# Kernel optimization log

Measured on AMD Instinct MI355X. Metric: run time of the kernel, lower is better.

## Reference

```python
import jax, jax.numpy as jnp
import numpy as np

EPS = 1e-6
LOG_2PI = float(np.log(2.0 * np.pi))


def setup_inputs() -> dict:
    key = jax.random.key(0)
    k1, k2 = jax.random.split(key)
    z = jax.random.normal(k1, (8, 32, 256, 256), dtype=jnp.float32)
    g = jax.random.uniform(k2, (8, 5, 256, 256), dtype=jnp.float32)
    return {"z": z, "g": g}


def _gmm_energy(z, g):
    b, c, h, w = z.shape
    k = g.shape[1]
    hw = h * w
    zf = z.reshape(b, c, hw)
    gf = g.reshape(b, k, hw)

    # phi: mean responsibility per component, [b, k]
    phi = jnp.sum(gf, axis=2) / hw

    # mu: weighted mean, then l2-normalized over channels, [b, k, c]
    gz = jnp.einsum('bkn,bcn->bkc', gf, zf)
    mu = gz / (jnp.sum(gf, axis=2, keepdims=True) + EPS)
    mu = mu / (EPS + jnp.linalg.norm(mu, axis=-1, keepdims=True))

    # centered data, [b, k, c, hw]
    z_mu = zf[:, None, :, :] - mu[..., None]

    # cov: in the source the g-weighting algebraically cancels
    # (sum(g)*M / sum(g) where M = z_mu @ z_mu.T), so cov = z_mu @ z_mu.T
    cov = jnp.einsum('bkcn,bkdn->bkcd', z_mu, z_mu)  # [b, k, c, c]
    # get_pd: add diag(clamp(diag, 1e-6)) (doubles the diagonal, floored)
    d = jnp.maximum(jnp.diagonal(cov, axis1=-2, axis2=-1), EPS)  # [b, k, c]
    cov = cov + jnp.eye(c, dtype=cov.dtype) * d[..., None, :]
    # l2norm over dims (0,1) of each [c,c] block = Frobenius normalization
    fro = jnp.sqrt(jnp.sum(cov * cov, axis=(-2, -1), keepdims=True))
    cov = cov / (EPS + fro)

    # energy: MVN log-prob of every pixel under each (b,k) Gaussian,
    # with phi (NOT log phi, faithful to source) added before logsumexp.
    L = jnp.linalg.cholesky(cov)  # [b, k, c, c]
    y = jax.scipy.linalg.solve_triangular(L, z_mu, lower=True)  # [b, k, c, hw]
    maha = jnp.sum(y * y, axis=2)  # [b, k, hw]
    logdet = 2.0 * jnp.sum(jnp.log(jnp.diagonal(L, axis1=-2, axis2=-1)), axis=-1)  # [b, k]
    log_prob = -0.5 * (c * LOG_2PI + maha) - 0.5 * logdet[..., None]  # [b, k, hw]
    weighted = log_prob + phi[..., None]
    log_sum = jax.scipy.special.logsumexp(weighted, axis=-1)  # [b, k]
    energy = -jnp.mean(log_sum) / hw
    return energy


def reference(z, g):
    return _gmm_energy(z, g)
```

## Files before the change

### kernel.cpp

```cpp
#include <hip/hip_runtime.h>
#include <math.h>

constexpr int B = 8, C = 32, K = 5, HW = 65536;
constexpr int K1B  = 64;
constexpr int K1PX = HW / K1B;
constexpr int NIT  = K1PX / 128;
constexpr int K3PX = 256;
constexpr int K3BLK = HW / K3PX;
constexpr int NPART = K3BLK * 4;
constexpr float NEG_HALF_C_LOG2PI_F = -29.406033062549518f;

typedef __attribute__((ext_vector_type(8))) short bf16x8;
typedef __attribute__((ext_vector_type(4))) float f32x4;

__device__ inline unsigned short f2bf(float f) {
  unsigned int u = __float_as_uint(f);
  return (unsigned short)((u + 0x7fffu + ((u >> 16) & 1u)) >> 16);
}
__device__ inline float bf2f(unsigned short h) {
  return __uint_as_float(((unsigned int)h) << 16);
}

__global__ __launch_bounds__(256) void k1_gram(const float* __restrict__ z,
                                               const float* __restrict__ g,
                                               float* __restrict__ part) {
  __shared__ __align__(16) unsigned short xs[96 * 136];
  unsigned int* xsu = (unsigned int*)xs;
  const int tid  = threadIdx.x;
  const int lane = tid & 63;
  const int w    = tid >> 6;
  const int b    = blockIdx.x / K1B;
  const int blk  = blockIdx.x % K1B;
  const int px0  = blk * K1PX;

  for (int idx = tid; idx < 22 * 64; idx += 256) {
    int rr  = idx >> 6;
    int row = (rr < 11) ? (37 + rr) : (85 + rr - 11);
    xsu[row * 68 + (idx & 63)] = (row == 37) ? 0x3f803f80u : 0u;
  }

  f32x4 a00 = {0.f,0.f,0.f,0.f}, a10 = {0.f,0.f,0.f,0.f}, a11 = {0.f,0.f,0.f,0.f};
  f32x4 a20 = {0.f,0.f,0.f,0.f}, a21 = {0.f,0.f,0.f,0.f}, a22 = {0.f,0.f,0.f,0.f};

  float2 pre[10];
#pragma unroll
  for (int j = 0; j < 10; ++j) {
    int r = w + 4 * j;
    if (r < 37) {
      const float* src = (r < 32) ? (z + (size_t)(b * C + r) * HW)
                                  : (g + (size_t)(b * K + (r - 32)) * HW);
      pre[j] = ((const float2*)(src + px0))[lane];
    }
  }

  const int lm = lane & 15, q = lane >> 4;
  const int co = w * 32 + q * 8;

  for (int it = 0; it < NIT; ++it) {
    __syncthreads();
#pragma unroll
    for (int j = 0; j < 10; ++j) {
      int r = w + 4 * j;
      if (r < 37) {
        unsigned short hx = f2bf(pre[j].x), hy = f2bf(pre[j].y);
        float lx = pre[j].x - bf2f(hx);
        float ly = pre[j].y - bf2f(hy);
        xsu[r * 68 + lane]        = (unsigned int)hx | ((unsigned int)hy << 16);
        xsu[(r + 48) * 68 + lane] = (unsigned int)f2bf(lx) | ((unsigned int)f2bf(ly) << 16);
      }
    }
    __syncthreads();
    if (it + 1 < NIT) {
#pragma unroll
      for (int j = 0; j < 10; ++j) {
        int r = w + 4 * j;
        if (r < 37) {
          const float* src = (r < 32) ? (z + (size_t)(b * C + r) * HW)
                                      : (g + (size_t)(b * K + (r - 32)) * HW);
          pre[j] = ((const float2*)(src + px0 + (it + 1) * 128))[lane];
        }
      }
    }
    bf16x8 f0h = *(const bf16x8*)&xs[(0  + lm) * 136 + co];
    bf16x8 f1h = *(const bf16x8*)&xs[(16 + lm) * 136 + co];
    bf16x8 f2h = *(const bf16x8*)&xs[(32 + lm) * 136 + co];
    bf16x8 f0l = *(const bf16x8*)&xs[(48 + lm) * 136 + co];
    bf16x8 f1l = *(const bf16x8*)&xs[(64 + lm) * 136 + co];
    bf16x8 f2l = *(const bf16x8*)&xs[(80 + lm) * 136 + co];
#define MF(d, x, y) d = __builtin_amdgcn_mfma_f32_16x16x32_bf16(x, y, d, 0, 0, 0)
    MF(a00, f0h, f0h); MF(a00, f0h, f0l); MF(a00, f0l, f0h);
    MF(a10, f1h, f0h); MF(a10, f1h, f0l); MF(a10, f1l, f0h);
    MF(a11, f1h, f1h); MF(a11, f1h, f1l); MF(a11, f1l, f1h);
    MF(a20, f2h, f0h); MF(a20, f2h, f0l); MF(a20, f2l, f0h);
    MF(a21, f2h, f1h); MF(a21, f2h, f1l); MF(a21, f2l, f1h);
    MF(a22, f2h, f2h); MF(a22, f2h, f2l); MF(a22, f2l, f2h);
#undef MF
  }

  __syncthreads();
  float* fb = (float*)xs;
#pragma unroll
  for (int rr = 0; rr < 4; ++rr) {
    fb[((w * 6 + 0) * 4 + rr) * 64 + lane] = a00[rr];
    fb[((w * 6 + 1) * 4 + rr) * 64 + lane] = a10[rr];
    fb[((w * 6 + 2) * 4 + rr) * 64 + lane] = a11[rr];
    fb[((w * 6 + 3) * 4 + rr) * 64 + lane] = a20[rr];
    fb[((w * 6 + 4) * 4 + rr) * 64 + lane] = a21[rr];
    fb[((w * 6 + 5) * 4 + rr) * 64 + lane] = a22[rr];
  }
  __syncthreads();
  float* po = part + (size_t)blockIdx.x * 1536;
#pragma unroll
  for (int t = 0; t < 6; ++t) {
    int sl = (tid >> 6), ln = (tid & 63);
    float v = fb[((0 * 6 + t) * 4 + sl) * 64 + ln] + fb[((1 * 6 + t) * 4 + sl) * 64 + ln]
            + fb[((2 * 6 + t) * 4 + sl) * 64 + ln] + fb[((3 * 6 + t) * 4 + sl) * 64 + ln];
    po[t * 256 + tid] = v;
  }
}

__global__ void k1b_reduce(const float* __restrict__ part, float* __restrict__ gram) {
  const int b = blockIdx.x / 6, t = blockIdx.x % 6;
  const int tid = threadIdx.x;
  const int rr = tid >> 6, lane = tid & 63;
  const int m = (lane >> 4) * 4 + rr, n = lane & 15;
  const int TI[6] = {0, 1, 1, 2, 2, 2};
  const int TJ[6] = {0, 0, 1, 0, 1, 2};
  double s = 0.0;
#pragma unroll 8
  for (int blk = 0; blk < K1B; ++blk)
    s += (double)part[(size_t)(b * K1B + blk) * 1536 + t * 256 + tid];
  int gr = TI[t] * 16 + m, gc = TJ[t] * 16 + n;
  if (gr < 40 && gc < 40) {
    gram[b * 1600 + gr * 40 + gc] = (float)s;
    gram[b * 1600 + gc * 40 + gr] = (float)s;
  }
}

__global__ __launch_bounds__(64) void k2_setup(const float* __restrict__ gram,
                                               unsigned short* __restrict__ ABout,
                                               float* __restrict__ vout,
                                               float* __restrict__ cterm) {
  const int b = blockIdx.x / K, k = blockIdx.x % K;
  const float* G = gram + b * 1600;
  const int lane = threadIdx.x;
  const int j32 = lane & 31;
  __shared__ float Amat[32][33];
  __shared__ float mus[32];

  const float sg = G[37 * 40 + 32 + k];
  float muj = G[(32 + k) * 40 + j32] / (sg + 1e-6f);
  const float szj = G[37 * 40 + j32];
  float nrm = muj * muj;
#pragma unroll
  for (int d = 1; d < 32; d <<= 1) nrm += __shfl_xor(nrm, d, 64);
  muj *= 1.f / (1e-6f + sqrtf(nrm));
  if (lane < 32) mus[lane] = muj;

  float col[32];
#pragma unroll
  for (int i = 0; i < 32; ++i) {
    const float mu_i = __shfl(muj, i, 64);
    const float sz_i = __shfl(szj, i, 64);
    float cv = G[i * 40 + j32] - mu_i * szj - muj * sz_i + 65536.f * mu_i * muj;
    if (i == lane) cv += fmaxf(cv, 1e-6f);
    col[i] = cv;
  }
  float fs = 0.f;
#pragma unroll
  for (int i = 0; i < 32; ++i) fs = fmaf(col[i], col[i], fs);
#pragma unroll
  for (int d = 1; d < 32; d <<= 1) fs += __shfl_xor(fs, d, 64);
  const float fsc = 1.f / (1e-6f + sqrtf(fs));
#pragma unroll
  for (int i = 0; i < 32; ++i) col[i] *= fsc;

  float sown = 0.f, dcap = 1.f;
#pragma unroll
  for (int j = 0; j < 32; ++j) {
    float dd = __shfl(col[j], j, 64);
    dd = fmaxf(dd, 1e-30f);
    const float s = 1.f / sqrtf(dd);
    if (lane == j) { sown = s; dcap = dd; }
    const float f = (lane > j) ? col[j] * s : 0.f;
#pragma unroll
    for (int i = j + 1; i < 32; ++i) {
      const float cji = __shfl(col[i], j, 64) * s;
      col[i] = fmaf(-cji, f, col[i]);
    }
  }

  float Lc[32];
#pragma unroll
  for (int i = 0; i < 32; ++i) Lc[i] = col[i] * sown;

  float x[32];
#pragma unroll
  for (int i = 0; i < 32; ++i) {
    float t0 = (lane == i) ? 1.f : 0.f, t1 = 0.f, t2 = 0.f, t3 = 0.f;
#pragma unroll
    for (int qq = 0; qq < i; ++qq) {
      const float lq = __shfl(Lc[i], qq, 64);
      const float p = lq * x[qq];
      if ((qq & 3) == 0) t0 -= p;
      else if ((qq & 3) == 1) t1 -= p;
      else if ((qq & 3) == 2) t2 -= p;
      else t3 -= p;
    }
    const float Lii = __shfl(Lc[i], i, 64);
    x[i] = ((t0 + t1) + (t2 + t3)) / Lii;
  }

  if (lane < 32) {
#pragma unroll
    for (int i = 0; i < 32; ++i) Amat[i][lane] = x[i];
  }
  __syncthreads();

  if (lane < 32) {
    float t = 0.f;
    for (int d2 = 0; d2 <= lane; ++d2) t = fmaf(Amat[lane][d2], mus[d2], t);
    vout[(b * K + k) * 32 + lane] = t;
  }

  float lg = 0.5f * logf(dcap);
#pragma unroll
  for (int d = 1; d < 32; d <<= 1) lg += __shfl_xor(lg, d, 64);
  if (lane == 0)
    cterm[b * K + k] = NEG_HALF_C_LOG2PI_F - lg + sg / 65536.f;

  unsigned short* Ao = ABout + (size_t)(b * K + k) * 2048;
#pragma unroll
  for (int e = lane; e < 1024; e += 64) {
    const int m = e >> 5, d2 = e & 31;
    const float a = Amat[m][d2];
    const unsigned int u = __float_as_uint(a);
    const float hf = __uint_as_float(u & 0xffff0000u);
    Ao[e] = (unsigned short)(u >> 16);
    Ao[1024 + e] = (unsigned short)(__float_as_uint(a - hf) >> 16);
  }
}

__global__ __launch_bounds__(256, 2) void k3_maha(const float* __restrict__ z,
                                                  const unsigned short* __restrict__ AB,
                                                  const float* __restrict__ vglob,
                                                  float2* __restrict__ partials) {
  __shared__ __align__(16) unsigned short zt[K3PX * 72];
  const int tid  = threadIdx.x;
  const int lane = tid & 63;
  const int w    = tid >> 6;
  const int b    = blockIdx.x / K3BLK;
  const int chb  = blockIdx.x % K3BLK;
  const int px0  = chb * K3PX;

  {
    const float* zb = z + (size_t)b * C * HW + px0 + 4 * lane;
    float4 rv[8];
#pragma unroll
    for (int i = 0; i < 8; ++i)
      rv[i] = *(const float4*)(zb + (size_t)(w * 8 + i) * HW);
#pragma unroll
    for (int p = 0; p < 4; ++p) {
      unsigned int hi[4], lo[4];
#pragma unroll
      for (int i = 0; i < 8; i += 2) {
        float a0 = (&rv[i].x)[p], a1 = (&rv[i + 1].x)[p];
        unsigned int u0 = __float_as_uint(a0), u1 = __float_as_uint(a1);
        float h0 = __uint_as_float(u0 & 0xffff0000u);
        float h1 = __uint_as_float(u1 & 0xffff0000u);
        hi[i >> 1] = (u0 >> 16) | (u1 & 0xffff0000u);
        lo[i >> 1] = (__float_as_uint(a0 - h0) >> 16) |
                     (__float_as_uint(a1 - h1) & 0xffff0000u);
      }
      unsigned int* row = (unsigned int*)&zt[(4 * lane + p) * 72];
      *(uint4*)(row + w * 4)      = make_uint4(hi[0], hi[1], hi[2], hi[3]);
      *(uint4*)(row + 16 + w * 4) = make_uint4(lo[0], lo[1], lo[2], lo[3]);
    }
  }
  __syncthreads();

  const int lm = lane & 15, q = lane >> 4;
  bf16x8 Ah[K][2], Al[K][2];
  f32x4 Ci[K][2];
#pragma unroll
  for (int k = 0; k < K; ++k) {
    const unsigned short* Abase = AB + (size_t)(b * K + k) * 2048;
    const float* vb = vglob + (size_t)(b * K + k) * 32;
#pragma unroll
    for (int mt = 0; mt < 2; ++mt) {
      const int m = mt * 16 + lm;
      Ah[k][mt] = *(const bf16x8*)(Abase + m * 32 + q * 8);
      Al[k][mt] = *(const bf16x8*)(Abase + 1024 + m * 32 + q * 8);
#pragma unroll
      for (int r = 0; r < 4; ++r)
        Ci[k][mt][r] = -vb[mt * 16 + q * 4 + r];
    }
  }

  float mm[K], ss[K];
#pragma unroll
  for (int k = 0; k < K; ++k) { mm[k] = -1e30f; ss[k] = 0.f; }

#pragma unroll
  for (int nt = 0; nt < 4; ++nt) {
    const int px = w * 64 + nt * 16 + lm;
    bf16x8 zh = *(const bf16x8*)&zt[px * 72 + q * 8];
    bf16x8 zl = *(const bf16x8*)&zt[px * 72 + 32 + q * 8];
#pragma unroll
    for (int k = 0; k < K; ++k) {
      float acc = 0.f;
#pragma unroll
      for (int mt = 0; mt < 2; ++mt) {
        f32x4 y = Ci[k][mt];
        y = __builtin_amdgcn_mfma_f32_16x16x32_bf16(Ah[k][mt], zh, y, 0, 0, 0);
        y = __builtin_amdgcn_mfma_f32_16x16x32_bf16(Ah[k][mt], zl, y, 0, 0, 0);
        y = __builtin_amdgcn_mfma_f32_16x16x32_bf16(Al[k][mt], zh, y, 0, 0, 0);
#pragma unroll
        for (int r = 0; r < 4; ++r) acc = fmaf(y[r], y[r], acc);
      }
      acc += __shfl_xor(acc, 16, 64);
      acc += __shfl_xor(acc, 32, 64);
      const float L = -0.5f * acc;
      const float nm = fmaxf(mm[k], L);
      ss[k] = ss[k] * __expf(mm[k] - nm) + __expf(L - nm);
      mm[k] = nm;
    }
  }
#pragma unroll
  for (int k = 0; k < K; ++k) {
#pragma unroll
    for (int d = 1; d < 16; d <<= 1) {
      float mo = __shfl_xor(mm[k], d, 64);
      float so = __shfl_xor(ss[k], d, 64);
      float nm = fmaxf(mm[k], mo);
      ss[k] = ss[k] * __expf(mm[k] - nm) + so * __expf(mo - nm);
      mm[k] = nm;
    }
    if (lane == 0)
      partials[((size_t)(b * K + k) * K3BLK + chb) * 4 + w] = make_float2(mm[k], ss[k]);
  }
}

__global__ void k4a_lse(const float2* __restrict__ partials,
                        const float* __restrict__ cterm,
                        float* __restrict__ lsebuf) {
  const int bk = blockIdx.x;
  const int lane = threadIdx.x;
  const float2* p = partials + (size_t)bk * NPART;
  float M = -1e30f, S = 0.f;
#pragma unroll 4
  for (int i = lane; i < NPART; i += 64) {
    const float2 qq = p[i];
    const float nm = fmaxf(M, qq.x);
    S = S * __expf(M - nm) + qq.y * __expf(qq.x - nm);
    M = nm;
  }
#pragma unroll
  for (int d = 1; d < 64; d <<= 1) {
    const float mo = __shfl_xor(M, d, 64);
    const float so = __shfl_xor(S, d, 64);
    const float nm = fmaxf(M, mo);
    S = S * __expf(M - nm) + so * __expf(mo - nm);
    M = nm;
  }
  if (lane == 0) lsebuf[bk] = M + logf(S) + cterm[bk];
}

__global__ void k4b_final(const float* __restrict__ lsebuf, float* __restrict__ out) {
  const int lane = threadIdx.x;
  double v = (lane < 40) ? (double)lsebuf[lane] : 0.0;
#pragma unroll
  for (int d = 1; d < 64; d <<= 1) v += __shfl_xor(v, d, 64);
  if (lane == 0) out[0] = (float)(-v / (40.0 * 65536.0));
}

extern "C" void kernel_launch(void* const* d_in, const int* in_sizes, int n_in,
                              void* d_out, int out_size, void* d_ws, size_t ws_size,
                              hipStream_t stream) {
  const float* z = (const float*)d_in[0];
  const float* g = (const float*)d_in[1];
  float* out = (float*)d_out;

  float2* part3 = (float2*)d_ws;
  float*  part1 = (float*)(part3 + 40 * NPART);
  float*  gram  = part1 + (B * K1B) * 1536;
  float*  vv    = gram + B * 1600;
  float*  ct    = vv + B * K * 32;
  float*  lsebuf = ct + B * K;
  unsigned short* AB = (unsigned short*)(lsebuf + 40);

  k1_gram<<<B * K1B, 256, 0, stream>>>(z, g, part1);
  k1b_reduce<<<B * 6, 256, 0, stream>>>(part1, gram);
  k2_setup<<<B * K, 64, 0, stream>>>(gram, AB, vv, ct);
  k3_maha<<<B * K3BLK, 256, 0, stream>>>(z, AB, vv, part3);
  k4a_lse<<<B * K, 64, 0, stream>>>(part3, ct, lsebuf);
  k4b_final<<<1, 64, 0, stream>>>(lsebuf, out);
}
```

Baseline: 171.8 us.

## Fuse setup kernels, drop z low-bf16 split, fuse final reduction with atomic counter

Merges the gram reduction and per-component Cholesky setup into one kernel per batch, with the gram kept in shared memory. It also merges the two final logsumexp kernels using a last-block atomic counter, removing two launches. In the Mahalanobis kernel, z is now stored only as a rounded bf16 value instead of a hi/lo split, which cuts one of three MFMAs per tile and halves the shared-memory tile. Dropping the z low part lowers the precision of the Mahalanobis distances. The setup stage now runs on only 8 blocks with serial per-element sums.

```diff
diff --git a/kernel.cpp b/kernel.cpp
--- a/kernel.cpp
+++ b/kernel.cpp
@@ -119,34 +119,46 @@
   }
 }
 
-__global__ void k1b_reduce(const float* __restrict__ part, float* __restrict__ gram) {
-  const int b = blockIdx.x / 6, t = blockIdx.x % 6;
+__global__ __launch_bounds__(512) void k12_setup(const float* __restrict__ part,
+                                                 unsigned short* __restrict__ ABout,
+                                                 float* __restrict__ vout,
+                                                 float* __restrict__ cterm,
+                                                 unsigned int* __restrict__ counter) {
+  const int b = blockIdx.x;
   const int tid = threadIdx.x;
-  const int rr = tid >> 6, lane = tid & 63;
-  const int m = (lane >> 4) * 4 + rr, n = lane & 15;
-  const int TI[6] = {0, 1, 1, 2, 2, 2};
-  const int TJ[6] = {0, 0, 1, 0, 1, 2};
-  double s = 0.0;
+  __shared__ float gram[1600];
+  __shared__ float AmatS[5][32][33];
+  __shared__ float musS[5][32];
+  if (b == 0 && tid == 0) *counter = 0u;
+
+  {
+    const int TI[6] = {0, 1, 1, 2, 2, 2};
+    const int TJ[6] = {0, 0, 1, 0, 1, 2};
+    for (int e = tid; e < 1536; e += 512) {
+      double s = 0.0;
 #pragma unroll 8
-  for (int blk = 0; blk < K1B; ++blk)
-    s += (double)part[(size_t)(b * K1B + blk) * 1536 + t * 256 + tid];
-  int gr = TI[t] * 16 + m, gc = TJ[t] * 16 + n;
-  if (gr < 40 && gc < 40) {
-    gram[b * 1600 + gr * 40 + gc] = (float)s;
-    gram[b * 1600 + gc * 40 + gr] = (float)s;
-  }
-}
-
-__global__ __launch_bounds__(64) void k2_setup(const float* __restrict__ gram,
-                                               unsigned short* __restrict__ ABout,
-                                               float* __restrict__ vout,
-                                               float* __restrict__ cterm) {
-  const int b = blockIdx.x / K, k = blockIdx.x % K;
-  const float* G = gram + b * 1600;
-  const int lane = threadIdx.x;
+      for (int blk = 0; blk < K1B; ++blk)
+        s += (double)part[(size_t)(b * K1B + blk) * 1536 + e];
+      const int t = e >> 8, idx = e & 255;
+      const int rr = idx >> 6, ln = idx & 63;
+      const int m = (ln >> 4) * 4 + rr, n = ln & 15;
+      const int gr = TI[t] * 16 + m, gc = TJ[t] * 16 + n;
+      if (gr < 40 && gc < 40) {
+        gram[gr * 40 + gc] = (float)s;
+        gram[gc * 40 + gr] = (float)s;
+      }
+    }
+  }
+  __syncthreads();
+
+  const int wv = tid >> 6;
+  if (wv >= 5) return;
+  const int k = wv;
+  const int lane = tid & 63;
   const int j32 = lane & 31;
-  __shared__ float Amat[32][33];
-  __shared__ float mus[32];
+  float (*Amat)[33] = AmatS[wv];
+  float* mus = musS[wv];
+  const float* G = gram;
 
   const float sg = G[37 * 40 + 32 + k];
   float muj = G[(32 + k) * 40 + j32] / (sg + 1e-6f);
@@ -215,7 +227,6 @@
 #pragma unroll
     for (int i = 0; i < 32; ++i) Amat[i][lane] = x[i];
   }
-  __syncthreads();
 
   if (lane < 32) {
     float t = 0.f;
@@ -241,11 +252,11 @@
   }
 }
 
-__global__ __launch_bounds__(256, 2) void k3_maha(const float* __restrict__ z,
-                                                  const unsigned short* __restrict__ AB,
-                                                  const float* __restrict__ vglob,
-                                                  float2* __restrict__ partials) {
-  __shared__ __align__(16) unsigned short zt[K3PX * 72];
+__global__ __launch_bounds__(256) void k3_maha(const float* __restrict__ z,
+                                               const unsigned short* __restrict__ AB,
+                                               const float* __restrict__ vglob,
+                                               float2* __restrict__ partials) {
+  __shared__ __align__(16) unsigned short zt[K3PX * 40];
   const int tid  = threadIdx.x;
   const int lane = tid & 63;
   const int w    = tid >> 6;
@@ -261,20 +272,13 @@
       rv[i] = *(const float4*)(zb + (size_t)(w * 8 + i) * HW);
 #pragma unroll
     for (int p = 0; p < 4; ++p) {
-      unsigned int hi[4], lo[4];
+      unsigned int hh[4];
 #pragma unroll
       for (int i = 0; i < 8; i += 2) {
-        float a0 = (&rv[i].x)[p], a1 = (&rv[i + 1].x)[p];
-        unsigned int u0 = __float_as_uint(a0), u1 = __float_as_uint(a1);
-        float h0 = __uint_as_float(u0 & 0xffff0000u);
-        float h1 = __uint_as_float(u1 & 0xffff0000u);
-        hi[i >> 1] = (u0 >> 16) | (u1 & 0xffff0000u);
-        lo[i >> 1] = (__float_as_uint(a0 - h0) >> 16) |
-                     (__float_as_uint(a1 - h1) & 0xffff0000u);
+        const float a0 = (&rv[i].x)[p], a1 = (&rv[i + 1].x)[p];
+        hh[i >> 1] = (unsigned int)f2bf(a0) | ((unsigned int)f2bf(a1) << 16);
       }
-      unsigned int* row = (unsigned int*)&zt[(4 * lane + p) * 72];
-      *(uint4*)(row + w * 4)      = make_uint4(hi[0], hi[1], hi[2], hi[3]);
-      *(uint4*)(row + 16 + w * 4) = make_uint4(lo[0], lo[1], lo[2], lo[3]);
+      *(uint4*)&zt[(4 * lane + p) * 40 + w * 8] = make_uint4(hh[0], hh[1], hh[2], hh[3]);
     }
   }
   __syncthreads();
@@ -304,8 +308,7 @@
 #pragma unroll
   for (int nt = 0; nt < 4; ++nt) {
     const int px = w * 64 + nt * 16 + lm;
-    bf16x8 zh = *(const bf16x8*)&zt[px * 72 + q * 8];
-    bf16x8 zl = *(const bf16x8*)&zt[px * 72 + 32 + q * 8];
+    bf16x8 zh = *(const bf16x8*)&zt[px * 40 + q * 8];
 #pragma unroll
     for (int k = 0; k < K; ++k) {
       float acc = 0.f;
@@ -313,7 +316,6 @@
       for (int mt = 0; mt < 2; ++mt) {
         f32x4 y = Ci[k][mt];
         y = __builtin_amdgcn_mfma_f32_16x16x32_bf16(Ah[k][mt], zh, y, 0, 0, 0);
-        y = __builtin_amdgcn_mfma_f32_16x16x32_bf16(Ah[k][mt], zl, y, 0, 0, 0);
         y = __builtin_amdgcn_mfma_f32_16x16x32_bf16(Al[k][mt], zh, y, 0, 0, 0);
 #pragma unroll
         for (int r = 0; r < 4; ++r) acc = fmaf(y[r], y[r], acc);
@@ -341,9 +343,11 @@
   }
 }
 
-__global__ void k4a_lse(const float2* __restrict__ partials,
-                        const float* __restrict__ cterm,
-                        float* __restrict__ lsebuf) {
+__global__ __launch_bounds__(64) void k4_final(const float2* __restrict__ partials,
+                                               const float* __restrict__ cterm,
+                                               float* __restrict__ lsebuf,
+                                               unsigned int* __restrict__ counter,
+                                               float* __restrict__ out) {
   const int bk = blockIdx.x;
   const int lane = threadIdx.x;
   const float2* p = partials + (size_t)bk * NPART;
@@ -363,15 +367,20 @@
     S = S * __expf(M - nm) + so * __expf(mo - nm);
     M = nm;
   }
-  if (lane == 0) lsebuf[bk] = M + logf(S) + cterm[bk];
-}
-
-__global__ void k4b_final(const float* __restrict__ lsebuf, float* __restrict__ out) {
-  const int lane = threadIdx.x;
-  double v = (lane < 40) ? (double)lsebuf[lane] : 0.0;
-#pragma unroll
-  for (int d = 1; d < 64; d <<= 1) v += __shfl_xor(v, d, 64);
-  if (lane == 0) out[0] = (float)(-v / (40.0 * 65536.0));
+  __shared__ int last;
+  if (lane == 0) {
+    atomicExch(&lsebuf[bk], M + logf(S) + cterm[bk]);
+    __threadfence();
+    last = (atomicAdd(counter, 1u) == 39u) ? 1 : 0;
+  }
+  __syncthreads();
+  if (last) {
+    const float v = (lane < 40) ? atomicAdd(&lsebuf[lane], 0.f) : 0.f;
+    double dv = (double)v;
+#pragma unroll
+    for (int d = 1; d < 64; d <<= 1) dv += __shfl_xor(dv, d, 64);
+    if (lane == 0) out[0] = (float)(-dv / (40.0 * 65536.0));
+  }
 }
 
 extern "C" void kernel_launch(void* const* d_in, const int* in_sizes, int n_in,
@@ -383,16 +392,14 @@
 
   float2* part3 = (float2*)d_ws;
   float*  part1 = (float*)(part3 + 40 * NPART);
-  float*  gram  = part1 + (B * K1B) * 1536;
-  float*  vv    = gram + B * 1600;
-  float*  ct    = vv + B * K * 32;
+  unsigned short* AB = (unsigned short*)(part1 + (size_t)(B * K1B) * 1536);
+  float*  vv     = (float*)(AB + 40 * 2048);
+  float*  ct     = vv + B * K * 32;
   float*  lsebuf = ct + B * K;
-  unsigned short* AB = (unsigned short*)(lsebuf + 40);
+  unsigned int* counter = (unsigned int*)(lsebuf + 40);
 
   k1_gram<<<B * K1B, 256, 0, stream>>>(z, g, part1);
-  k1b_reduce<<<B * 6, 256, 0, stream>>>(part1, gram);
-  k2_setup<<<B * K, 64, 0, stream>>>(gram, AB, vv, ct);
+  k12_setup<<<B, 512, 0, stream>>>(part1, AB, vv, ct, counter);
   k3_maha<<<B * K3BLK, 256, 0, stream>>>(z, AB, vv, part3);
-  k4a_lse<<<B * K, 64, 0, stream>>>(part3, ct, lsebuf);
-  k4b_final<<<1, 64, 0, stream>>>(lsebuf, out);
-}
+  k4_final<<<B * K, 64, 0, stream>>>(part3, ct, lsebuf, counter, out);
+}
```

Result: slower. 279.3 us (+62.6%).
